# Kernel tuning notes

Hardware: AMD Instinct MI355X
Metric: run time of the kernel (lower is better)

The kernel has to match this reference:

```python
import jax, jax.numpy as jnp
import numpy as np

H, D = 16, 64  # num_heads, head_dim (hidden = H*D = 1024)
EPS = 1e-6

def elu_plus_one(x):
    return jax.nn.elu(x) + 1.0

def setup_inputs() -> dict:
    key = jax.random.key(0)
    ks = jax.random.split(key, 12)
    hid = H * D
    s = 0.02
    return {
        "hidden_states": jax.random.normal(ks[0], (1, 2048, hid), jnp.float32),
        "w_q": jax.random.normal(ks[1], (hid, hid), jnp.float32) * s,
        "w_k": jax.random.normal(ks[2], (hid, hid), jnp.float32) * s,
        "w_v": jax.random.normal(ks[3], (hid, hid), jnp.float32) * s,
        "w_o": jax.random.normal(ks[4], (hid, hid), jnp.float32) * s,
        "memory_gate": jnp.zeros((H,), jnp.float32),
        "eg_w1": jax.random.normal(ks[5], (hid, hid // 4), jnp.float32) * s,
        "eg_b1": jnp.zeros((hid // 4,), jnp.float32),
        "eg_w2": jax.random.normal(ks[6], (hid // 4, 1), jnp.float32) * s,
        "eg_b2": jnp.zeros((1,), jnp.float32),
        "fine_mem": jax.random.normal(ks[7], (4, H, D, D), jnp.float32) * s,
        "fine_norm": jax.random.uniform(ks[8], (4, H, D), jnp.float32),
    }

def _retrieve(sigma_q, memory, memory_norm):
    # sigma_q: [b,h,s,d], memory: [h,d,e], memory_norm: [h,d]
    a = jnp.einsum('bhsd,hde->bhse', sigma_q, memory)
    relevance = jnp.einsum('bhsd,hd->bhs', sigma_q, memory_norm)
    out = a / jnp.clip(relevance, EPS, None)[..., None]
    return out, relevance

def reference(hidden_states, w_q, w_k, w_v, w_o, memory_gate,
              eg_w1, eg_b1, eg_w2, eg_b2, fine_mem, fine_norm):
    B, S, hid = hidden_states.shape
    def proj(w):
        return (hidden_states @ w).reshape(B, S, H, D).transpose(0, 2, 1, 3)  # [b,h,s,d]
    q, k, v = proj(w_q), proj(w_k), proj(w_v)
    sigma_q = elu_plus_one(q)

    # coarse memory = sum of fine memories
    M_coarse = fine_mem.sum(0)        # [h,d,d]
    z_coarse = fine_norm.sum(0)       # [h,d]
    output_coarse, _ = _retrieve(sigma_q, M_coarse, z_coarse)  # [b,h,s,d]

    # learned expansion gate on coarse representation
    coarse_repr = output_coarse.transpose(0, 2, 1, 3).reshape(B, S, hid)
    logit = jax.nn.relu(coarse_repr @ eg_w1 + eg_b1) @ eg_w2 + eg_b2  # [b,s,1]
    expansion_prob = jax.nn.sigmoid(logit)                            # [b,s,1]

    # fine-grained retrieval: attention-weighted mix over the 4 banks
    outs = jnp.einsum('bhsd,fhde->fbhse', sigma_q, fine_mem)   # [f,b,h,s,d]
    rels = jnp.einsum('bhsd,fhd->fbhs', sigma_q, fine_norm)    # [f,b,h,s]
    outs = outs / jnp.clip(rels, EPS, None)[..., None]
    weights = jax.nn.softmax(rels.mean(-1), axis=0)            # [f,b,h]
    output_fine = (outs * weights[:, :, :, None, None]).sum(0)  # [b,h,s,d]

    ep = expansion_prob.transpose(0, 2, 1)[..., None]          # [b,1,s,1]
    memory_output = ep * output_fine + (1.0 - ep) * output_coarse

    # causal linear attention within current segment
    sigma_k = elu_plus_one(k)
    kv = jnp.einsum('bhsd,bhse->bhsde', sigma_k, v)            # [b,h,s,d,d]
    kv_cumsum = jnp.cumsum(kv, axis=2)
    k_cumsum = jnp.cumsum(sigma_k, axis=2)
    num = jnp.einsum('bhsd,bhsde->bhse', sigma_q, kv_cumsum)
    den = jnp.clip(jnp.einsum('bhsd,bhsd->bhs', sigma_q, k_cumsum), EPS, None)[..., None]
    local_output = num / den

    gate = jax.nn.sigmoid(memory_gate).reshape(1, H, 1, 1)
    output = gate * memory_output + (1.0 - gate) * local_output
    output = output.transpose(0, 2, 1, 3).reshape(B, S, hid)
    return output @ w_o
```

## Files before the change

kernel.cpp:

```cpp
#include <hip/hip_runtime.h>
#include <cmath>

#define EPSF 1e-6f
#define LDK 72


typedef __attribute__((ext_vector_type(8))) short bf16x8;
typedef __attribute__((ext_vector_type(4))) float f32x4;
typedef __attribute__((ext_vector_type(8))) unsigned short u16x8;

__device__ __forceinline__ float wave_allsum(float v) {
#pragma unroll
  for (int off = 32; off > 0; off >>= 1) v += __shfl_xor(v, off, 64);
  return v;
}

__device__ __forceinline__ unsigned short f2bf(float f) {
  unsigned int u = __float_as_uint(f);
  unsigned int r = (u + 0x7fffu + ((u >> 16) & 1u)) >> 16;
  return (unsigned short)r;
}
__device__ __forceinline__ float bf2f(unsigned short u) {
  return __uint_as_float(((unsigned int)u) << 16);
}

__global__ __launch_bounds__(256) void k0_mcT(const float* __restrict__ FM,
    const float* __restrict__ FN, unsigned short* __restrict__ MCT,
    float* __restrict__ ZC)
{
  int h = blockIdx.x, tid = threadIdx.x;
  __shared__ float tile[64][65];
  for (int i = tid; i < 4096; i += 256) {
    int dp = i >> 6, e = i & 63;
    float s = FM[(0 * 16 + h) * 4096 + i] + FM[(1 * 16 + h) * 4096 + i]
            + FM[(2 * 16 + h) * 4096 + i] + FM[(3 * 16 + h) * 4096 + i];
    tile[dp][e] = s;
  }
  if (tid < 64)
    ZC[h * 64 + tid] = FN[h * 64 + tid] + FN[1024 + h * 64 + tid]
                     + FN[2048 + h * 64 + tid] + FN[3072 + h * 64 + tid];
  __syncthreads();
  for (int i = tid; i < 4096; i += 256) {
    int e = i >> 6, dp = i & 63;
    MCT[h * 4096 + e * 64 + dp] = f2bf(tile[dp][e]);
  }
}

__global__ __launch_bounds__(256) void cast_bf16_k(const float* __restrict__ X,
    unsigned short* __restrict__ Y)
{
  int i = blockIdx.x * 256 + threadIdx.x;
  float4 v = *reinterpret_cast<const float4*>(X + i * 4);
  ushort4 o; o.x = f2bf(v.x); o.y = f2bf(v.y); o.z = f2bf(v.z); o.w = f2bf(v.w);
  *reinterpret_cast<ushort4*>(Y + i * 4) = o;
}

__global__ __launch_bounds__(256) void cast_transpose_k(const float* __restrict__ W,
    unsigned short* __restrict__ WT, int N)
{
  __shared__ float tile[64][65];
  int n0 = blockIdx.x * 64, k0 = blockIdx.y * 64;
  int tid = threadIdx.x;
  for (int i = tid; i < 4096; i += 256) {
    int r = i >> 6, c = i & 63;
    tile[r][c] = W[(k0 + r) * N + n0 + c];
  }
  __syncthreads();
  for (int i = tid; i < 1024; i += 256) {
    int r = i >> 4, c4 = (i & 15) * 4;
    ushort4 o;
    o.x = f2bf(tile[c4 + 0][r]); o.y = f2bf(tile[c4 + 1][r]);
    o.z = f2bf(tile[c4 + 2][r]); o.w = f2bf(tile[c4 + 3][r]);
    *reinterpret_cast<ushort4*>(&WT[(n0 + r) * 1024 + k0 + c4]) = o;
  }
}

__global__ __launch_bounds__(256) void cast_w4(const float* __restrict__ W0,
    const float* __restrict__ W1, const float* __restrict__ W2, const float* __restrict__ W3,
    unsigned short* __restrict__ T0, unsigned short* __restrict__ T1,
    unsigned short* __restrict__ T2, unsigned short* __restrict__ T3)
{
  int z = blockIdx.z;
  const float* W = (z == 0) ? W0 : (z == 1) ? W1 : (z == 2) ? W2 : W3;
  unsigned short* WT = (z == 0) ? T0 : (z == 1) ? T1 : (z == 2) ? T2 : T3;
  __shared__ float tile[64][65];
  int n0 = blockIdx.x * 64, k0 = blockIdx.y * 64;
  int tid = threadIdx.x;
  for (int i = tid; i < 4096; i += 256) {
    int r = i >> 6, c = i & 63;
    tile[r][c] = W[(k0 + r) * 1024 + n0 + c];
  }
  __syncthreads();
  for (int i = tid; i < 1024; i += 256) {
    int r = i >> 4, c4 = (i & 15) * 4;
    ushort4 o;
    o.x = f2bf(tile[c4 + 0][r]); o.y = f2bf(tile[c4 + 1][r]);
    o.z = f2bf(tile[c4 + 2][r]); o.w = f2bf(tile[c4 + 3][r]);
    *reinterpret_cast<ushort4*>(&WT[(n0 + r) * 1024 + k0 + c4]) = o;
  }
}

__global__ __launch_bounds__(256) void fm_cast_t(const float* __restrict__ FM,
    unsigned short* __restrict__ FMT)
{
  __shared__ float tile[64][65];
  int b = blockIdx.x, tid = threadIdx.x;
  const float* src = FM + b * 4096;
  for (int i = tid; i < 4096; i += 256) tile[i >> 6][i & 63] = src[i];
  __syncthreads();
  unsigned short* dst = FMT + b * 4096;
  for (int i = tid; i < 4096; i += 256) {
    int e = i >> 6, dp = i & 63;
    dst[e * 64 + dp] = f2bf(tile[dp][e]);
  }
}

__global__ __launch_bounds__(256) void mm_bf16(const unsigned short* __restrict__ A,
    const unsigned short* __restrict__ BT, float* __restrict__ C, int ldc, int act)
{
  __shared__ unsigned short As[128 * LDK];
  __shared__ unsigned short Bs[128 * LDK];
  int tid = threadIdx.x;
  int m0 = blockIdx.y * 128, n0 = blockIdx.x * 128;
  int wid = tid >> 6, lane = tid & 63;
  int wr = wid >> 1, wc = wid & 1;
  int lr = lane & 15, lg = lane >> 4;

  f32x4 acc[4][4];
#pragma unroll
  for (int m = 0; m < 4; ++m)
#pragma unroll
    for (int n = 0; n < 4; ++n)
#pragma unroll
      for (int r = 0; r < 4; ++r) acc[m][n][r] = 0.f;

  for (int kt = 0; kt < 16; ++kt) {
    int k0 = kt * 64;
#pragma unroll
    for (int p = 0; p < 4; ++p) {
      int c = p * 256 + tid;
      int row = c >> 3, k8 = c & 7;
      u16x8 va = *reinterpret_cast<const u16x8*>(A + (m0 + row) * 1024 + k0 + k8 * 8);
      *reinterpret_cast<u16x8*>(&As[row * LDK + k8 * 8]) = va;
      u16x8 vb = *reinterpret_cast<const u16x8*>(BT + (n0 + row) * 1024 + k0 + k8 * 8);
      *reinterpret_cast<u16x8*>(&Bs[row * LDK + k8 * 8]) = vb;
    }
    __syncthreads();
#pragma unroll
    for (int kk = 0; kk < 2; ++kk) {
      bf16x8 af[4], bfr[4];
#pragma unroll
      for (int m = 0; m < 4; ++m)
        af[m] = *reinterpret_cast<const bf16x8*>(&As[(wr * 64 + m * 16 + lr) * LDK + kk * 32 + lg * 8]);
#pragma unroll
      for (int n = 0; n < 4; ++n)
        bfr[n] = *reinterpret_cast<const bf16x8*>(&Bs[(wc * 64 + n * 16 + lr) * LDK + kk * 32 + lg * 8]);
#pragma unroll
      for (int m = 0; m < 4; ++m)
#pragma unroll
        for (int n = 0; n < 4; ++n)
          acc[m][n] = __builtin_amdgcn_mfma_f32_16x16x32_bf16(af[m], bfr[n], acc[m][n], 0, 0, 0);
    }
    __syncthreads();
  }
#pragma unroll
  for (int m = 0; m < 4; ++m)
#pragma unroll
    for (int n = 0; n < 4; ++n)
#pragma unroll
      for (int r = 0; r < 4; ++r) {
        float v = acc[m][n][r];
        if (act) v = v > 0.f ? v + 1.f : expf(v);
        C[(m0 + wr * 64 + m * 16 + lg * 4 + r) * ldc + n0 + wc * 64 + n * 16 + lr] = v;
      }
}

__global__ __launch_bounds__(256) void proj_bf16(const unsigned short* __restrict__ A,
    const unsigned short* __restrict__ WqT, const unsigned short* __restrict__ WkT,
    const unsigned short* __restrict__ WvT,
    unsigned short* __restrict__ Oq, unsigned short* __restrict__ Ok,
    unsigned short* __restrict__ Ov)
{
  int z = blockIdx.z;
  const unsigned short* BT = (z == 0) ? WqT : (z == 1) ? WkT : WvT;
  unsigned short* C = (z == 0) ? Oq : (z == 1) ? Ok : Ov;

  __shared__ unsigned short As[128 * LDK];
  __shared__ unsigned short Bs[128 * LDK];
  int tid = threadIdx.x;
  int m0 = blockIdx.y * 128, n0 = blockIdx.x * 128;
  int wid = tid >> 6, lane = tid & 63;
  int wr = wid >> 1, wc = wid & 1;
  int lr = lane & 15, lg = lane >> 4;
  int act = (z < 2) ? 1 : 0;

  f32x4 acc[4][4];
#pragma unroll
  for (int m = 0; m < 4; ++m)
#pragma unroll
    for (int n = 0; n < 4; ++n)
#pragma unroll
      for (int r = 0; r < 4; ++r) acc[m][n][r] = 0.f;

  for (int kt = 0; kt < 16; ++kt) {
    int k0 = kt * 64;
#pragma unroll
    for (int p = 0; p < 4; ++p) {
      int c = p * 256 + tid;
      int row = c >> 3, k8 = c & 7;
      u16x8 va = *reinterpret_cast<const u16x8*>(A + (m0 + row) * 1024 + k0 + k8 * 8);
      *reinterpret_cast<u16x8*>(&As[row * LDK + k8 * 8]) = va;
      u16x8 vb = *reinterpret_cast<const u16x8*>(BT + (n0 + row) * 1024 + k0 + k8 * 8);
      *reinterpret_cast<u16x8*>(&Bs[row * LDK + k8 * 8]) = vb;
    }
    __syncthreads();
#pragma unroll
    for (int kk = 0; kk < 2; ++kk) {
      bf16x8 af[4], bfr[4];
#pragma unroll
      for (int m = 0; m < 4; ++m)
        af[m] = *reinterpret_cast<const bf16x8*>(&As[(wr * 64 + m * 16 + lr) * LDK + kk * 32 + lg * 8]);
#pragma unroll
      for (int n = 0; n < 4; ++n)
        bfr[n] = *reinterpret_cast<const bf16x8*>(&Bs[(wc * 64 + n * 16 + lr) * LDK + kk * 32 + lg * 8]);
#pragma unroll
      for (int m = 0; m < 4; ++m)
#pragma unroll
        for (int n = 0; n < 4; ++n)
          acc[m][n] = __builtin_amdgcn_mfma_f32_16x16x32_bf16(af[m], bfr[n], acc[m][n], 0, 0, 0);
    }
    __syncthreads();
  }
#pragma unroll
  for (int m = 0; m < 4; ++m)
#pragma unroll
    for (int n = 0; n < 4; ++n)
#pragma unroll
      for (int r = 0; r < 4; ++r) {
        float v = acc[m][n][r];
        if (act) v = v > 0.f ? v + 1.f : expf(v);
        C[(m0 + wr * 64 + m * 16 + lg * 4 + r) * 1024 + n0 + wc * 64 + n * 16 + lr] = f2bf(v);
      }
}

__global__ __launch_bounds__(256) void eg_fin(const float* __restrict__ H1,
    const float* __restrict__ B1, const float* __restrict__ W2,
    const float* __restrict__ B2, float* __restrict__ EP)
{
  int wid = threadIdx.x >> 6, lane = threadIdx.x & 63;
  int s = blockIdx.x * 4 + wid;
  float4 h = *reinterpret_cast<const float4*>(H1 + s * 256 + lane * 4);
  float4 b = *reinterpret_cast<const float4*>(B1 + lane * 4);
  float4 w = *reinterpret_cast<const float4*>(W2 + lane * 4);
  float v = fmaxf(h.x + b.x, 0.f) * w.x + fmaxf(h.y + b.y, 0.f) * w.y
          + fmaxf(h.z + b.z, 0.f) * w.z + fmaxf(h.w + b.w, 0.f) * w.w;
  v = wave_allsum(v);
  if (lane == 0) EP[s] = 1.f / (1.f + expf(-(v + B2[0])));
}

__global__ __launch_bounds__(256) void rels_kernel(const unsigned short* __restrict__ SQB,
    const float* __restrict__ ZC, const float* __restrict__ FN,
    float* __restrict__ RELC, float* __restrict__ RELS, float* __restrict__ PARTS)
{
  int h = blockIdx.x, st = blockIdx.y, tid = threadIdx.x;
  int s0 = st * 64;
  __shared__ float sqT[64][68];
  __shared__ float zf[5][64];
  __shared__ float relb[5][64];
#pragma unroll
  for (int p = 0; p < 2; ++p) {
    int cidx = p * 256 + tid;
    int r = cidx >> 3, d8 = cidx & 7;
    u16x8 v = *reinterpret_cast<const u16x8*>(SQB + (s0 + r) * 1024 + h * 64 + d8 * 8);
#pragma unroll
    for (int j = 0; j < 8; ++j) sqT[d8 * 8 + j][r] = bf2f((unsigned short)v[j]);
  }
  for (int idx = tid; idx < 320; idx += 256) {
    int w = idx >> 6, d = idx & 63;
    zf[w][d] = (w == 0) ? ZC[h * 64 + d] : FN[(w - 1) * 1024 + h * 64 + d];
  }
  __syncthreads();
  {
    int s = tid & 63, wh = tid >> 6;
    float r = 0.f;
    for (int dp = 0; dp < 64; ++dp) r += sqT[dp][s] * zf[wh][dp];
    relb[wh][s] = r;
    if (wh == 0) {
      float r4 = 0.f;
      for (int dp = 0; dp < 64; ++dp) r4 += sqT[dp][s] * zf[4][dp];
      relb[4][s] = r4;
    }
  }
  __syncthreads();
  if (tid < 64) {
    RELC[h * 2048 + s0 + tid] = relb[0][tid];
#pragma unroll
    for (int f = 0; f < 4; ++f)
      RELS[f * 32768 + h * 2048 + s0 + tid] = relb[1 + f][tid];
#pragma unroll
    for (int f = 0; f < 4; ++f) {
      float v = wave_allsum(relb[1 + f][tid]);
      if (tid == 0) PARTS[f * 512 + h * 32 + st] = v;
    }
  }
}

__global__ __launch_bounds__(256) void coarse_mfma(const unsigned short* __restrict__ SQB,
    const unsigned short* __restrict__ MCT, const float* __restrict__ RELC,
    unsigned short* __restrict__ COB)
{
  int h = blockIdx.x, st = blockIdx.y, tid = threadIdx.x;
  int w = tid >> 6, lane = tid & 63, lr = lane & 15, lg = lane >> 4;
  int s0 = st * 128;
  __shared__ unsigned short A_lds[128 * LDK];
  __shared__ unsigned short B_lds[64 * LDK];
#pragma unroll
  for (int p = 0; p < 4; ++p) {
    int c = p * 256 + tid;
    int row = c >> 3, k8 = c & 7;
    *reinterpret_cast<u16x8*>(&A_lds[row * LDK + k8 * 8]) =
        *reinterpret_cast<const u16x8*>(SQB + (s0 + row) * 1024 + h * 64 + k8 * 8);
  }
#pragma unroll
  for (int p = 0; p < 2; ++p) {
    int c = p * 256 + tid;
    int e = c >> 3, k8 = c & 7;
    *reinterpret_cast<u16x8*>(&B_lds[e * LDK + k8 * 8]) =
        *reinterpret_cast<const u16x8*>(MCT + h * 4096 + e * 64 + k8 * 8);
  }
  __syncthreads();

  f32x4 acc[2][4];
#pragma unroll
  for (int m = 0; m < 2; ++m)
#pragma unroll
    for (int n = 0; n < 4; ++n)
#pragma unroll
      for (int r = 0; r < 4; ++r) acc[m][n][r] = 0.f;

#pragma unroll
  for (int kk = 0; kk < 2; ++kk) {
    bf16x8 af[2], bfr[4];
#pragma unroll
    for (int m = 0; m < 2; ++m)
      af[m] = *reinterpret_cast<const bf16x8*>(&A_lds[(w * 32 + m * 16 + lr) * LDK + kk * 32 + lg * 8]);
#pragma unroll
    for (int n = 0; n < 4; ++n)
      bfr[n] = *reinterpret_cast<const bf16x8*>(&B_lds[(n * 16 + lr) * LDK + kk * 32 + lg * 8]);
#pragma unroll
    for (int m = 0; m < 2; ++m)
#pragma unroll
      for (int n = 0; n < 4; ++n)
        acc[m][n] = __builtin_amdgcn_mfma_f32_16x16x32_bf16(af[m], bfr[n], acc[m][n], 0, 0, 0);
  }
#pragma unroll
  for (int m = 0; m < 2; ++m)
#pragma unroll
    for (int r = 0; r < 4; ++r) {
      int s = s0 + w * 32 + m * 16 + lg * 4 + r;
      float rc = fmaxf(RELC[h * 2048 + s], EPSF);
#pragma unroll
      for (int n = 0; n < 4; ++n)
        COB[s * 1024 + h * 64 + n * 16 + lr] = f2bf(acc[m][n][r] / rc);
    }
}

__global__ void weights_kernel(const float* __restrict__ P, float* __restrict__ W)
{
  int h = threadIdx.x;
  if (h >= 16) return;
  float r[4];
#pragma unroll
  for (int f = 0; f < 4; ++f) {
    float s = 0.f;
    for (int t = 0; t < 32; ++t) s += P[f * 512 + h * 32 + t];
    r[f] = s * (1.f / 2048.f);
  }
  float m = fmaxf(fmaxf(r[0], r[1]), fmaxf(r[2], r[3]));
  float e0 = expf(r[0] - m), e1 = expf(r[1] - m), e2 = expf(r[2] - m), e3 = expf(r[3] - m);
  float inv = 1.f / (e0 + e1 + e2 + e3);
  W[0 * 16 + h] = e0 * inv; W[1 * 16 + h] = e1 * inv;
  W[2 * 16 + h] = e2 * inv; W[3 * 16 + h] = e3 * inv;
}

__global__ __launch_bounds__(256) void fine_mfma(const unsigned short* __restrict__ SQB,
    const unsigned short* __restrict__ FMT, const float* __restrict__ RELS,
    const float* __restrict__ WT, const float* __restrict__ EP,
    const unsigned short* __restrict__ COB, float* __restrict__ MO)
{
  int h = blockIdx.x, st = blockIdx.y;
  int tid = threadIdx.x;
  int w = tid >> 6, lane = tid & 63;
  int lr = lane & 15, lg = lane >> 4;
  int s0 = st * 128;

  __shared__ unsigned short A_lds[128 * LDK];
  __shared__ unsigned short B_lds[4 * 64 * LDK];
  __shared__ float w4s[4];
  if (tid < 4) w4s[tid] = WT[tid * 16 + h];

#pragma unroll
  for (int p = 0; p < 4; ++p) {
    int c = p * 256 + tid;
    int row = c >> 3, k8 = c & 7;
    *reinterpret_cast<u16x8*>(&A_lds[row * LDK + k8 * 8]) =
        *reinterpret_cast<const u16x8*>(SQB + (s0 + row) * 1024 + h * 64 + k8 * 8);
  }
#pragma unroll
  for (int p = 0; p < 8; ++p) {
    int c = p * 256 + tid;
    int f = c >> 9, rem = c & 511;
    int e = rem >> 3, k8 = rem & 7;
    *reinterpret_cast<u16x8*>(&B_lds[(f * 64 + e) * LDK + k8 * 8]) =
        *reinterpret_cast<const u16x8*>(FMT + (f * 16 + h) * 4096 + e * 64 + k8 * 8);
  }
  __syncthreads();

  f32x4 acc[4][2][4];
#pragma unroll
  for (int f = 0; f < 4; ++f)
#pragma unroll
    for (int m = 0; m < 2; ++m)
#pragma unroll
      for (int n = 0; n < 4; ++n)
#pragma unroll
        for (int r = 0; r < 4; ++r) acc[f][m][n][r] = 0.f;

#pragma unroll
  for (int kk = 0; kk < 2; ++kk) {
    bf16x8 af[2];
#pragma unroll
    for (int m = 0; m < 2; ++m)
      af[m] = *reinterpret_cast<const bf16x8*>(&A_lds[(w * 32 + m * 16 + lr) * LDK + kk * 32 + lg * 8]);
#pragma unroll
    for (int f = 0; f < 4; ++f) {
      bf16x8 bf4[4];
#pragma unroll
      for (int n = 0; n < 4; ++n)
        bf4[n] = *reinterpret_cast<const bf16x8*>(&B_lds[(f * 64 + n * 16 + lr) * LDK + kk * 32 + lg * 8]);
#pragma unroll
      for (int m = 0; m < 2; ++m)
#pragma unroll
        for (int n = 0; n < 4; ++n)
          acc[f][m][n] = __builtin_amdgcn_mfma_f32_16x16x32_bf16(af[m], bf4[n], acc[f][m][n], 0, 0, 0);
    }
  }

#pragma unroll
  for (int m = 0; m < 2; ++m)
#pragma unroll
    for (int r = 0; r < 4; ++r) {
      int s = s0 + w * 32 + m * 16 + lg * 4 + r;
      float e = EP[s];
      float i0 = w4s[0] / fmaxf(RELS[0 * 32768 + h * 2048 + s], EPSF);
      float i1 = w4s[1] / fmaxf(RELS[1 * 32768 + h * 2048 + s], EPSF);
      float i2 = w4s[2] / fmaxf(RELS[2 * 32768 + h * 2048 + s], EPSF);
      float i3 = w4s[3] / fmaxf(RELS[3 * 32768 + h * 2048 + s], EPSF);
#pragma unroll
      for (int n = 0; n < 4; ++n) {
        int dg = h * 64 + n * 16 + lr;
        float fine = acc[0][m][n][r] * i0 + acc[1][m][n][r] * i1
                   + acc[2][m][n][r] * i2 + acc[3][m][n][r] * i3;
        float cv = bf2f(COB[s * 1024 + dg]);
        MO[s * 1024 + dg] = e * fine + (1.f - e) * cv;
      }
    }
}

__global__ __launch_bounds__(256) void chunk_mfma(const unsigned short* __restrict__ SKB,
    const unsigned short* __restrict__ VVB, float* __restrict__ ST)
{
  int h = blockIdx.x, c = blockIdx.y, tid = threadIdx.x;
  int w = tid >> 6, lane = tid & 63, lr = lane & 15, lg = lane >> 4;
  int sb = c * 64;
  __shared__ unsigned short A_lds[64 * LDK];
  __shared__ unsigned short B_lds[80 * LDK];
#pragma unroll
  for (int p = 0; p < 2; ++p) {
    int cc = p * 256 + tid;
    int t = cc >> 3, e8 = cc & 7;
    u16x8 kv = *reinterpret_cast<const u16x8*>(SKB + (sb + t) * 1024 + h * 64 + e8 * 8);
    u16x8 vv = *reinterpret_cast<const u16x8*>(VVB + (sb + t) * 1024 + h * 64 + e8 * 8);
#pragma unroll
    for (int j = 0; j < 8; ++j) {
      A_lds[(e8 * 8 + j) * LDK + t] = (unsigned short)kv[j];
      B_lds[(e8 * 8 + j) * LDK + t] = (unsigned short)vv[j];
    }
  }
  if (tid < 64) B_lds[64 * LDK + tid] = 0x3F80;
  for (int i = tid; i < 15 * 64; i += 256) {
    int row = 65 + (i >> 6), col = i & 63;
    B_lds[row * LDK + col] = 0;
  }
  __syncthreads();

  f32x4 acc[5];
#pragma unroll
  for (int n = 0; n < 5; ++n)
#pragma unroll
    for (int r = 0; r < 4; ++r) acc[n][r] = 0.f;
#pragma unroll
  for (int kk = 0; kk < 2; ++kk) {
    bf16x8 af = *reinterpret_cast<const bf16x8*>(&A_lds[(w * 16 + lr) * LDK + kk * 32 + lg * 8]);
#pragma unroll
    for (int n = 0; n < 5; ++n) {
      bf16x8 bfr = *reinterpret_cast<const bf16x8*>(&B_lds[(n * 16 + lr) * LDK + kk * 32 + lg * 8]);
      acc[n] = __builtin_amdgcn_mfma_f32_16x16x32_bf16(af, bfr, acc[n], 0, 0, 0);
    }
  }
  float* base = ST + (h * 32 + c) * 4160;
#pragma unroll
  for (int r = 0; r < 4; ++r) {
    int d = w * 16 + lg * 4 + r;
#pragma unroll
    for (int n = 0; n < 4; ++n)
      base[d * 64 + n * 16 + lr] = acc[n][r];
    if (lr == 0) base[4096 + d] = acc[4][r];
  }
}

__global__ __launch_bounds__(256) void scan_kernel(const float* __restrict__ ST,
    unsigned short* __restrict__ STB)
{
  int gidx = blockIdx.x * 256 + threadIdx.x;
  int h = gidx / 4160, idx = gidx - h * 4160;
  if (h >= 16) return;
  float run = 0.f;
#pragma unroll 4
  for (int c = 0; c < 32; ++c) {
    float t = ST[(h * 32 + c) * 4160 + idx];
    STB[(h * 32 + c) * 4160 + idx] = f2bf(run);
    run += t;
  }
}

__global__ __launch_bounds__(256) void lattn_mfma(const unsigned short* __restrict__ SQB,
    const unsigned short* __restrict__ SKB, const unsigned short* __restrict__ VVB,
    const unsigned short* __restrict__ STB, float* __restrict__ OUT)
{
  int h = blockIdx.x, c = blockIdx.y, tid = threadIdx.x;
  int w = tid >> 6, lane = tid & 63, lr = lane & 15, lg = lane >> 4;
  int sb = c * 64;
  const unsigned short* stb = STB + (h * 32 + c) * 4160;

  __shared__ unsigned short A_lds[64 * LDK];
  __shared__ unsigned short K_lds[64 * LDK];
  __shared__ unsigned short P_lds[80 * LDK];
  __shared__ unsigned short V_lds[80 * LDK];
  __shared__ unsigned short S_lds[64 * LDK];

#pragma unroll
  for (int p = 0; p < 2; ++p) {
    int cc = p * 256 + tid;
    int row = cc >> 3, k8 = cc & 7;
    *reinterpret_cast<u16x8*>(&A_lds[row * LDK + k8 * 8]) =
        *reinterpret_cast<const u16x8*>(SQB + (sb + row) * 1024 + h * 64 + k8 * 8);
    *reinterpret_cast<u16x8*>(&K_lds[row * LDK + k8 * 8]) =
        *reinterpret_cast<const u16x8*>(SKB + (sb + row) * 1024 + h * 64 + k8 * 8);
  }
  for (int i = tid; i < 4096; i += 256) {
    int d = i >> 6, e = i & 63;
    P_lds[e * LDK + d] = stb[i];
  }
#pragma unroll
  for (int p = 0; p < 2; ++p) {
    int cc = p * 256 + tid;
    int t = cc >> 3, e8 = cc & 7;
    u16x8 v = *reinterpret_cast<const u16x8*>(VVB + (sb + t) * 1024 + h * 64 + e8 * 8);
#pragma unroll
    for (int j = 0; j < 8; ++j) V_lds[(e8 * 8 + j) * LDK + t] = (unsigned short)v[j];
  }
  if (tid < 64) {
    P_lds[64 * LDK + tid] = stb[4096 + tid];
    V_lds[64 * LDK + tid] = 0x3F80;
  }
  for (int i = tid; i < 15 * 64; i += 256) {
    int row = 65 + (i >> 6), col = i & 63;
    P_lds[row * LDK + col] = 0;
    V_lds[row * LDK + col] = 0;
  }
  __syncthreads();

  f32x4 acc_i[5];
#pragma unroll
  for (int n = 0; n < 5; ++n)
#pragma unroll
    for (int r = 0; r < 4; ++r) acc_i[n][r] = 0.f;
#pragma unroll
  for (int kk = 0; kk < 2; ++kk) {
    bf16x8 af = *reinterpret_cast<const bf16x8*>(&A_lds[(w * 16 + lr) * LDK + kk * 32 + lg * 8]);
#pragma unroll
    for (int n = 0; n < 5; ++n) {
      bf16x8 bfr = *reinterpret_cast<const bf16x8*>(&P_lds[(n * 16 + lr) * LDK + kk * 32 + lg * 8]);
      acc_i[n] = __builtin_amdgcn_mfma_f32_16x16x32_bf16(af, bfr, acc_i[n], 0, 0, 0);
    }
  }
  f32x4 acc_s[4];
#pragma unroll
  for (int n = 0; n < 4; ++n)
#pragma unroll
    for (int r = 0; r < 4; ++r) acc_s[n][r] = 0.f;
#pragma unroll
  for (int kk = 0; kk < 2; ++kk) {
    bf16x8 af = *reinterpret_cast<const bf16x8*>(&A_lds[(w * 16 + lr) * LDK + kk * 32 + lg * 8]);
#pragma unroll
    for (int n = 0; n < 4; ++n) {
      bf16x8 bfr = *reinterpret_cast<const bf16x8*>(&K_lds[(n * 16 + lr) * LDK + kk * 32 + lg * 8]);
      acc_s[n] = __builtin_amdgcn_mfma_f32_16x16x32_bf16(af, bfr, acc_s[n], 0, 0, 0);
    }
  }
#pragma unroll
  for (int n = 0; n < 4; ++n)
#pragma unroll
    for (int r = 0; r < 4; ++r) {
      int s_loc = w * 16 + lg * 4 + r, t = n * 16 + lr;
      float v = (t <= s_loc) ? acc_s[n][r] : 0.f;
      S_lds[s_loc * LDK + t] = f2bf(v);
    }
  __syncthreads();
  f32x4 acc_p[5];
#pragma unroll
  for (int n = 0; n < 5; ++n)
#pragma unroll
    for (int r = 0; r < 4; ++r) acc_p[n][r] = 0.f;
#pragma unroll
  for (int kk = 0; kk < 2; ++kk) {
    bf16x8 af = *reinterpret_cast<const bf16x8*>(&S_lds[(w * 16 + lr) * LDK + kk * 32 + lg * 8]);
#pragma unroll
    for (int n = 0; n < 5; ++n) {
      bf16x8 bfr = *reinterpret_cast<const bf16x8*>(&V_lds[(n * 16 + lr) * LDK + kk * 32 + lg * 8]);
      acc_p[n] = __builtin_amdgcn_mfma_f32_16x16x32_bf16(af, bfr, acc_p[n], 0, 0, 0);
    }
  }
#pragma unroll
  for (int r = 0; r < 4; ++r) {
    float den = acc_i[4][r] + acc_p[4][r];
    den = __shfl(den, lane & 48);
    den = fmaxf(den, EPSF);
    int s = sb + w * 16 + lg * 4 + r;
#pragma unroll
    for (int n = 0; n < 4; ++n)
      OUT[s * 1024 + h * 64 + n * 16 + lr] = (acc_i[n][r] + acc_p[n][r]) / den;
  }
}

__global__ __launch_bounds__(256) void combine_bf16(const float* __restrict__ MO,
    const float* __restrict__ LO, const float* __restrict__ MG,
    unsigned short* __restrict__ CBB)
{
  int i = blockIdx.x * 256 + threadIdx.x;
  float4 m4 = *reinterpret_cast<const float4*>(MO + i * 4);
  float4 l4 = *reinterpret_cast<const float4*>(LO + i * 4);
  int hh = ((i * 4) >> 6) & 15;
  float g = 1.f / (1.f + expf(-MG[hh]));
  ushort4 o;
  o.x = f2bf(g * m4.x + (1.f - g) * l4.x);
  o.y = f2bf(g * m4.y + (1.f - g) * l4.y);
  o.z = f2bf(g * m4.z + (1.f - g) * l4.z);
  o.w = f2bf(g * m4.w + (1.f - g) * l4.w);
  *reinterpret_cast<ushort4*>(CBB + i * 4) = o;
}

extern "C" void kernel_launch(void* const* d_in, const int* in_sizes, int n_in,
                              void* d_out, int out_size, void* d_ws, size_t ws_size,
                              hipStream_t stream)
{
  const float* hs   = (const float*)d_in[0];
  const float* wq   = (const float*)d_in[1];
  const float* wk   = (const float*)d_in[2];
  const float* wv   = (const float*)d_in[3];
  const float* wo   = (const float*)d_in[4];
  const float* mg   = (const float*)d_in[5];
  const float* egw1 = (const float*)d_in[6];
  const float* egb1 = (const float*)d_in[7];
  const float* egw2 = (const float*)d_in[8];
  const float* egb2 = (const float*)d_in[9];
  const float* fm   = (const float*)d_in[10];
  const float* fn   = (const float*)d_in[11];
  float* out = (float*)d_out;

  float* ws     = (float*)d_ws;
  float* mo     = ws;
  float* lo     = mo + 2097152;
  float* zc     = lo + 2097152;
  float* rels   = zc + 1024;
  float* parts  = rels + 131072;
  float* wts    = parts + 2048;
  float* ep     = wts + 64;
  float* relc   = ep + 2048;
  float* states = relc + 32768;
  float* h1     = states + 2129920;
  unsigned short* hsb  = (unsigned short*)(h1 + 524288);
  unsigned short* sqb  = hsb + 2097152;
  unsigned short* skb  = sqb + 2097152;
  unsigned short* vvb  = skb + 2097152;
  unsigned short* cob  = vvb + 2097152;
  unsigned short* cbb  = cob + 2097152;
  unsigned short* wqT  = cbb + 2097152;
  unsigned short* wkT  = wqT + 1048576;
  unsigned short* wvT  = wkT + 1048576;
  unsigned short* woT  = wvT + 1048576;
  unsigned short* w1T  = woT + 1048576;
  unsigned short* fmbT = w1T + 262144;
  unsigned short* mcT  = fmbT + 262144;
  unsigned short* statesb = mcT + 65536;

  k0_mcT<<<16, 256, 0, stream>>>(fm, fn, mcT, zc);
  cast_w4<<<dim3(16, 16, 4), 256, 0, stream>>>(wq, wk, wv, wo, wqT, wkT, wvT, woT);
  cast_transpose_k<<<dim3(4, 16), 256, 0, stream>>>(egw1, w1T, 256);
  fm_cast_t<<<64, 256, 0, stream>>>(fm, fmbT);
  cast_bf16_k<<<2048, 256, 0, stream>>>(hs, hsb);
  proj_bf16<<<dim3(8, 16, 3), 256, 0, stream>>>(hsb, wqT, wkT, wvT, sqb, skb, vvb);
  rels_kernel<<<dim3(16, 32), 256, 0, stream>>>(sqb, zc, fn, relc, rels, parts);
  coarse_mfma<<<dim3(16, 16), 256, 0, stream>>>(sqb, mcT, relc, cob);
  mm_bf16<<<dim3(2, 16), 256, 0, stream>>>(cob, w1T, h1, 256, 0);
  eg_fin<<<512, 256, 0, stream>>>(h1, egb1, egw2, egb2, ep);
  weights_kernel<<<1, 64, 0, stream>>>(parts, wts);
  fine_mfma<<<dim3(16, 16), 256, 0, stream>>>(sqb, fmbT, rels, wts, ep, cob, mo);
  chunk_mfma<<<dim3(16, 32), 256, 0, stream>>>(skb, vvb, states);
  scan_kernel<<<260, 256, 0, stream>>>(states, statesb);
  lattn_mfma<<<dim3(16, 32), 256, 0, stream>>>(sqb, skb, vvb, statesb, lo);
  combine_bf16<<<2048, 256, 0, stream>>>(mo, lo, mg, cbb);
  mm_bf16<<<dim3(8, 16), 256, 0, stream>>>(cbb, woT, out, 1024, 0);
}
```

Before: 143.3 us.

## Fuse gate-combine into output GEMM, fold softmax weights into fine kernel

The memory and local outputs are now written as bf16 instead of fp32. The sigmoid-gated combine moves into the A-tile load of a new output-projection GEMM, which removes the combine kernel and its fp32 round trip. The tiny weights_kernel launch is dropped: each fine_mfma block computes the bank softmax from the partial sums itself. k0_mcT is also split over 4x more blocks for parallelism. The cost is redundant combine work across the 8 N-tile blocks of the GEMM and an extra bf16 rounding before the gate mix.

```diff
diff --git a/kernel.cpp b/kernel.cpp
--- a/kernel.cpp
+++ b/kernel.cpp
@@ -28,21 +28,22 @@
     const float* __restrict__ FN, unsigned short* __restrict__ MCT,
     float* __restrict__ ZC)
 {
-  int h = blockIdx.x, tid = threadIdx.x;
-  __shared__ float tile[64][65];
-  for (int i = tid; i < 4096; i += 256) {
-    int dp = i >> 6, e = i & 63;
-    float s = FM[(0 * 16 + h) * 4096 + i] + FM[(1 * 16 + h) * 4096 + i]
-            + FM[(2 * 16 + h) * 4096 + i] + FM[(3 * 16 + h) * 4096 + i];
-    tile[dp][e] = s;
-  }
-  if (tid < 64)
+  int h = blockIdx.x, q = blockIdx.y, tid = threadIdx.x;
+  __shared__ float tile[16][65];
+  for (int i = tid; i < 1024; i += 256) {
+    int dpl = i >> 6, e = i & 63;
+    int idx = (q * 16 + dpl) * 64 + e;
+    float s = FM[(0 * 16 + h) * 4096 + idx] + FM[(1 * 16 + h) * 4096 + idx]
+            + FM[(2 * 16 + h) * 4096 + idx] + FM[(3 * 16 + h) * 4096 + idx];
+    tile[dpl][e] = s;
+  }
+  if (q == 0 && tid < 64)
     ZC[h * 64 + tid] = FN[h * 64 + tid] + FN[1024 + h * 64 + tid]
                      + FN[2048 + h * 64 + tid] + FN[3072 + h * 64 + tid];
   __syncthreads();
-  for (int i = tid; i < 4096; i += 256) {
-    int e = i >> 6, dp = i & 63;
-    MCT[h * 4096 + e * 64 + dp] = f2bf(tile[dp][e]);
+  for (int i = tid; i < 1024; i += 256) {
+    int e = i >> 4, dpl = i & 15;
+    MCT[h * 4096 + e * 64 + q * 16 + dpl] = f2bf(tile[dpl][e]);
   }
 }
 
@@ -175,6 +176,74 @@
       }
 }
 
+__global__ __launch_bounds__(256) void mm_gate_bf16(const unsigned short* __restrict__ MOB,
+    const unsigned short* __restrict__ LOB, const float* __restrict__ MG,
+    const unsigned short* __restrict__ BT, float* __restrict__ C)
+{
+  __shared__ unsigned short As[128 * LDK];
+  __shared__ unsigned short Bs[128 * LDK];
+  __shared__ float gs[16];
+  int tid = threadIdx.x;
+  int m0 = blockIdx.y * 128, n0 = blockIdx.x * 128;
+  int wid = tid >> 6, lane = tid & 63;
+  int wr = wid >> 1, wc = wid & 1;
+  int lr = lane & 15, lg = lane >> 4;
+  if (tid < 16) gs[tid] = 1.f / (1.f + expf(-MG[tid]));
+  __syncthreads();
+
+  f32x4 acc[4][4];
+#pragma unroll
+  for (int m = 0; m < 4; ++m)
+#pragma unroll
+    for (int n = 0; n < 4; ++n)
+#pragma unroll
+      for (int r = 0; r < 4; ++r) acc[m][n][r] = 0.f;
+
+  for (int kt = 0; kt < 16; ++kt) {
+    int k0 = kt * 64;
+#pragma unroll
+    for (int p = 0; p < 4; ++p) {
+      int c = p * 256 + tid;
+      int row = c >> 3, k8 = c & 7;
+      int col = k0 + k8 * 8;
+      float g = gs[col >> 6];
+      u16x8 mv = *reinterpret_cast<const u16x8*>(MOB + (m0 + row) * 1024 + col);
+      u16x8 lv = *reinterpret_cast<const u16x8*>(LOB + (m0 + row) * 1024 + col);
+      u16x8 o;
+#pragma unroll
+      for (int j = 0; j < 8; ++j)
+        o[j] = f2bf(g * bf2f((unsigned short)mv[j]) + (1.f - g) * bf2f((unsigned short)lv[j]));
+      *reinterpret_cast<u16x8*>(&As[row * LDK + k8 * 8]) = o;
+      u16x8 vb = *reinterpret_cast<const u16x8*>(BT + (n0 + row) * 1024 + k0 + k8 * 8);
+      *reinterpret_cast<u16x8*>(&Bs[row * LDK + k8 * 8]) = vb;
+    }
+    __syncthreads();
+#pragma unroll
+    for (int kk = 0; kk < 2; ++kk) {
+      bf16x8 af[4], bfr[4];
+#pragma unroll
+      for (int m = 0; m < 4; ++m)
+        af[m] = *reinterpret_cast<const bf16x8*>(&As[(wr * 64 + m * 16 + lr) * LDK + kk * 32 + lg * 8]);
+#pragma unroll
+      for (int n = 0; n < 4; ++n)
+        bfr[n] = *reinterpret_cast<const bf16x8*>(&Bs[(wc * 64 + n * 16 + lr) * LDK + kk * 32 + lg * 8]);
+#pragma unroll
+      for (int m = 0; m < 4; ++m)
+#pragma unroll
+        for (int n = 0; n < 4; ++n)
+          acc[m][n] = __builtin_amdgcn_mfma_f32_16x16x32_bf16(af[m], bfr[n], acc[m][n], 0, 0, 0);
+    }
+    __syncthreads();
+  }
+#pragma unroll
+  for (int m = 0; m < 4; ++m)
+#pragma unroll
+    for (int n = 0; n < 4; ++n)
+#pragma unroll
+      for (int r = 0; r < 4; ++r)
+        C[(m0 + wr * 64 + m * 16 + lg * 4 + r) * 1024 + n0 + wc * 64 + n * 16 + lr] = acc[m][n][r];
+}
+
 __global__ __launch_bounds__(256) void proj_bf16(const unsigned short* __restrict__ A,
     const unsigned short* __restrict__ WqT, const unsigned short* __restrict__ WkT,
     const unsigned short* __restrict__ WvT,
@@ -365,28 +434,10 @@
     }
 }
 
-__global__ void weights_kernel(const float* __restrict__ P, float* __restrict__ W)
-{
-  int h = threadIdx.x;
-  if (h >= 16) return;
-  float r[4];
-#pragma unroll
-  for (int f = 0; f < 4; ++f) {
-    float s = 0.f;
-    for (int t = 0; t < 32; ++t) s += P[f * 512 + h * 32 + t];
-    r[f] = s * (1.f / 2048.f);
-  }
-  float m = fmaxf(fmaxf(r[0], r[1]), fmaxf(r[2], r[3]));
-  float e0 = expf(r[0] - m), e1 = expf(r[1] - m), e2 = expf(r[2] - m), e3 = expf(r[3] - m);
-  float inv = 1.f / (e0 + e1 + e2 + e3);
-  W[0 * 16 + h] = e0 * inv; W[1 * 16 + h] = e1 * inv;
-  W[2 * 16 + h] = e2 * inv; W[3 * 16 + h] = e3 * inv;
-}
-
 __global__ __launch_bounds__(256) void fine_mfma(const unsigned short* __restrict__ SQB,
     const unsigned short* __restrict__ FMT, const float* __restrict__ RELS,
-    const float* __restrict__ WT, const float* __restrict__ EP,
-    const unsigned short* __restrict__ COB, float* __restrict__ MO)
+    const float* __restrict__ PARTS, const float* __restrict__ EP,
+    const unsigned short* __restrict__ COB, unsigned short* __restrict__ MOB)
 {
   int h = blockIdx.x, st = blockIdx.y;
   int tid = threadIdx.x;
@@ -396,8 +447,12 @@
 
   __shared__ unsigned short A_lds[128 * LDK];
   __shared__ unsigned short B_lds[4 * 64 * LDK];
-  __shared__ float w4s[4];
-  if (tid < 4) w4s[tid] = WT[tid * 16 + h];
+  __shared__ float rmean[4];
+  if (tid < 4) {
+    float s = 0.f;
+    for (int t = 0; t < 32; ++t) s += PARTS[tid * 512 + h * 32 + t];
+    rmean[tid] = s * (1.f / 2048.f);
+  }
 
 #pragma unroll
   for (int p = 0; p < 4; ++p) {
@@ -446,23 +501,29 @@
     }
   }
 
+  float rm = fmaxf(fmaxf(rmean[0], rmean[1]), fmaxf(rmean[2], rmean[3]));
+  float e0 = expf(rmean[0] - rm), e1 = expf(rmean[1] - rm);
+  float e2 = expf(rmean[2] - rm), e3 = expf(rmean[3] - rm);
+  float winv = 1.f / (e0 + e1 + e2 + e3);
+  float w0 = e0 * winv, w1 = e1 * winv, w2 = e2 * winv, w3 = e3 * winv;
+
 #pragma unroll
   for (int m = 0; m < 2; ++m)
 #pragma unroll
     for (int r = 0; r < 4; ++r) {
       int s = s0 + w * 32 + m * 16 + lg * 4 + r;
       float e = EP[s];
-      float i0 = w4s[0] / fmaxf(RELS[0 * 32768 + h * 2048 + s], EPSF);
-      float i1 = w4s[1] / fmaxf(RELS[1 * 32768 + h * 2048 + s], EPSF);
-      float i2 = w4s[2] / fmaxf(RELS[2 * 32768 + h * 2048 + s], EPSF);
-      float i3 = w4s[3] / fmaxf(RELS[3 * 32768 + h * 2048 + s], EPSF);
+      float i0 = w0 / fmaxf(RELS[0 * 32768 + h * 2048 + s], EPSF);
+      float i1 = w1 / fmaxf(RELS[1 * 32768 + h * 2048 + s], EPSF);
+      float i2 = w2 / fmaxf(RELS[2 * 32768 + h * 2048 + s], EPSF);
+      float i3 = w3 / fmaxf(RELS[3 * 32768 + h * 2048 + s], EPSF);
 #pragma unroll
       for (int n = 0; n < 4; ++n) {
         int dg = h * 64 + n * 16 + lr;
         float fine = acc[0][m][n][r] * i0 + acc[1][m][n][r] * i1
                    + acc[2][m][n][r] * i2 + acc[3][m][n][r] * i3;
         float cv = bf2f(COB[s * 1024 + dg]);
-        MO[s * 1024 + dg] = e * fine + (1.f - e) * cv;
+        MOB[s * 1024 + dg] = f2bf(e * fine + (1.f - e) * cv);
       }
     }
 }
@@ -536,7 +597,7 @@
 
 __global__ __launch_bounds__(256) void lattn_mfma(const unsigned short* __restrict__ SQB,
     const unsigned short* __restrict__ SKB, const unsigned short* __restrict__ VVB,
-    const unsigned short* __restrict__ STB, float* __restrict__ OUT)
+    const unsigned short* __restrict__ STB, unsigned short* __restrict__ LOB)
 {
   int h = blockIdx.x, c = blockIdx.y, tid = threadIdx.x;
   int w = tid >> 6, lane = tid & 63, lr = lane & 15, lg = lane >> 4;
@@ -640,25 +701,8 @@
     int s = sb + w * 16 + lg * 4 + r;
 #pragma unroll
     for (int n = 0; n < 4; ++n)
-      OUT[s * 1024 + h * 64 + n * 16 + lr] = (acc_i[n][r] + acc_p[n][r]) / den;
-  }
-}
-
-__global__ __launch_bounds__(256) void combine_bf16(const float* __restrict__ MO,
-    const float* __restrict__ LO, const float* __restrict__ MG,
-    unsigned short* __restrict__ CBB)
-{
-  int i = blockIdx.x * 256 + threadIdx.x;
-  float4 m4 = *reinterpret_cast<const float4*>(MO + i * 4);
-  float4 l4 = *reinterpret_cast<const float4*>(LO + i * 4);
-  int hh = ((i * 4) >> 6) & 15;
-  float g = 1.f / (1.f + expf(-MG[hh]));
-  ushort4 o;
-  o.x = f2bf(g * m4.x + (1.f - g) * l4.x);
-  o.y = f2bf(g * m4.y + (1.f - g) * l4.y);
-  o.z = f2bf(g * m4.z + (1.f - g) * l4.z);
-  o.w = f2bf(g * m4.w + (1.f - g) * l4.w);
-  *reinterpret_cast<ushort4*>(CBB + i * 4) = o;
+      LOB[s * 1024 + h * 64 + n * 16 + lr] = f2bf((acc_i[n][r] + acc_p[n][r]) / den);
+  }
 }
 
 extern "C" void kernel_launch(void* const* d_in, const int* in_sizes, int n_in,
@@ -680,13 +724,10 @@
   float* out = (float*)d_out;
 
   float* ws     = (float*)d_ws;
-  float* mo     = ws;
-  float* lo     = mo + 2097152;
-  float* zc     = lo + 2097152;
+  float* zc     = ws;
   float* rels   = zc + 1024;
   float* parts  = rels + 131072;
-  float* wts    = parts + 2048;
-  float* ep     = wts + 64;
+  float* ep     = parts + 2048;
   float* relc   = ep + 2048;
   float* states = relc + 32768;
   float* h1     = states + 2129920;
@@ -695,8 +736,9 @@
   unsigned short* skb  = sqb + 2097152;
   unsigned short* vvb  = skb + 2097152;
   unsigned short* cob  = vvb + 2097152;
-  unsigned short* cbb  = cob + 2097152;
-  unsigned short* wqT  = cbb + 2097152;
+  unsigned short* mob  = cob + 2097152;
+  unsigned short* lob  = mob + 2097152;
+  unsigned short* wqT  = lob + 2097152;
   unsigned short* wkT  = wqT + 1048576;
   unsigned short* wvT  = wkT + 1048576;
   unsigned short* woT  = wvT + 1048576;
@@ -705,7 +747,7 @@
   unsigned short* mcT  = fmbT + 262144;
   unsigned short* statesb = mcT + 65536;
 
-  k0_mcT<<<16, 256, 0, stream>>>(fm, fn, mcT, zc);
+  k0_mcT<<<dim3(16, 4), 256, 0, stream>>>(fm, fn, mcT, zc);
   cast_w4<<<dim3(16, 16, 4), 256, 0, stream>>>(wq, wk, wv, wo, wqT, wkT, wvT, woT);
   cast_transpose_k<<<dim3(4, 16), 256, 0, stream>>>(egw1, w1T, 256);
   fm_cast_t<<<64, 256, 0, stream>>>(fm, fmbT);
@@ -715,11 +757,9 @@
   coarse_mfma<<<dim3(16, 16), 256, 0, stream>>>(sqb, mcT, relc, cob);
   mm_bf16<<<dim3(2, 16), 256, 0, stream>>>(cob, w1T, h1, 256, 0);
   eg_fin<<<512, 256, 0, stream>>>(h1, egb1, egw2, egb2, ep);
-  weights_kernel<<<1, 64, 0, stream>>>(parts, wts);
-  fine_mfma<<<dim3(16, 16), 256, 0, stream>>>(sqb, fmbT, rels, wts, ep, cob, mo);
+  fine_mfma<<<dim3(16, 16), 256, 0, stream>>>(sqb, fmbT, rels, parts, ep, cob, mob);
   chunk_mfma<<<dim3(16, 32), 256, 0, stream>>>(skb, vvb, states);
   scan_kernel<<<260, 256, 0, stream>>>(states, statesb);
-  lattn_mfma<<<dim3(16, 32), 256, 0, stream>>>(sqb, skb, vvb, statesb, lo);
-  combine_bf16<<<2048, 256, 0, stream>>>(mo, lo, mg, cbb);
-  mm_bf16<<<dim3(8, 16), 256, 0, stream>>>(cbb, woT, out, 1024, 0);
-}
+  lattn_mfma<<<dim3(16, 32), 256, 0, stream>>>(sqb, skb, vvb, statesb, lob);
+  mm_gate_bf16<<<dim3(8, 16), 256, 0, stream>>>(mob, lob, mg, woT, out);
+}
```

New measurement: 142.1 us. Within noise of the previous version (-0.9%).
